# Kernel optimization log

Hardware: AMD Instinct MI355X
Metric: run time of the kernel (lower is better)

Reference implementation:

```python
import jax, jax.numpy as jnp
import numpy as np

NX, NY, NZ = 432, 496, 1
D = 64        # num_pt_features
K = 3         # NUM_K
M = 1024      # memory size
BEV = 128     # num_bev_features
NCOORD = 3
NV = 10000    # pillars in scene
NP = 16384    # points in scene
BN_EPS = 1e-3
SHRINK = 0.0025


def hard_shrink_relu(x, lambd, eps=1e-12):
    return jax.nn.relu(x - lambd) * x / (jnp.abs(x - lambd) + eps)


def batchnorm_train(x, gamma, beta, eps=BN_EPS):
    # torch BatchNorm1d training-mode math (biased variance)
    mu = jnp.mean(x, axis=0)
    var = jnp.mean((x - mu) ** 2, axis=0)
    return (x - mu) * jax.lax.rsqrt(var + eps) * gamma + beta


def pdist2(a, b, eps=1e-5):
    # sqrt(eps + |  ||a||^2 + ||b||^2 - 2 a.b |), shape [n1, n2]
    n1 = jnp.sum(a * a, axis=1, keepdims=True)
    n2 = jnp.sum(b * b, axis=1, keepdims=True)
    d2 = n1 + n2.T - 2.0 * (a @ b.T)
    return jnp.sqrt(eps + jnp.abs(d2))


def memory_lookup(x_flat, mem_w, shrink):
    # MemAE-style memory unit: softmax addressing + hard shrink + L1 renorm
    att = jax.nn.softmax(x_flat @ mem_w.T, axis=1)          # [N, M]
    att = hard_shrink_relu(att, shrink)
    att = att / jnp.maximum(jnp.sum(jnp.abs(att), axis=1, keepdims=True), 1e-12)
    return att @ mem_w                                       # [N, D]


def setup_inputs() -> dict:
    key = jax.random.key(0)
    ks = jax.random.split(key, 8)
    rng = np.random.default_rng(0)
    flat = rng.choice(NX * NY, size=NV, replace=False)       # unique BEV cells
    x = (flat % NX).astype(np.int32)
    y = (flat // NX).astype(np.int32)
    coords = jnp.asarray(np.stack([np.zeros(NV, np.int32), x, y,
                                   np.zeros(NV, np.int32)], axis=1))  # (b, x, y, z)
    pc = jax.random.uniform(ks[1], (NP, 4), dtype=jnp.float32)
    point_coords = pc * jnp.array([0.0, NX, NY, 1.0], dtype=jnp.float32)
    return {
        "pillar_features": jax.random.normal(ks[0], (NV, D), dtype=jnp.float32),
        "coords": coords,
        "point_features": jax.random.normal(ks[2], (NP, D), dtype=jnp.float32),
        "point_coords": point_coords,
        "adapt_w": jax.random.normal(ks[3], (BEV // 2, D * K), dtype=jnp.float32) * 0.05,
        "bn1_g": jnp.ones((BEV // 2,), dtype=jnp.float32),
        "bn1_b": jnp.zeros((BEV // 2,), dtype=jnp.float32),
        "weight_w": jax.random.normal(ks[4], (2, BEV // 2), dtype=jnp.float32) * 0.1,
        "bn2_g": jnp.ones((2,), dtype=jnp.float32),
        "bn2_b": jnp.zeros((2,), dtype=jnp.float32),
        "mem_w": jax.random.normal(ks[5], (M, D), dtype=jnp.float32) * 0.1,
    }


def reference(pillar_features, coords, point_features, point_coords,
              adapt_w, bn1_g, bn1_b, weight_w, bn2_g, bn2_b, mem_w):
    nv = pillar_features.shape[0]
    pillars = pillar_features.T                              # [D, nv]

    # --- coord-based retrieval: smallest-K pdist(pillar coords, point coords) ---
    dist = pdist2(coords.astype(jnp.float32), point_coords)  # [nv, np]
    _, idx_c = jax.lax.top_k(-dist, K)                       # [nv, K]
    pillars_positive_coord = point_features[idx_c]           # [nv, K, D]

    # --- feature-based retrieval: top-K of softmax(points @ pillars, axis=0) ---
    score = jax.nn.softmax(point_features @ pillars, axis=0) # [np, nv]
    _, idx_f = jax.lax.top_k(score.T, K)                     # [nv, K]
    points_positive = point_features[idx_f]                  # [nv, K, D]

    # --- memory unit on both branches ---
    out_f = memory_lookup(points_positive.reshape(nv * K, D), mem_w, SHRINK).reshape(nv, K * D)
    out_c = memory_lookup(pillars_positive_coord.reshape(nv * K, D), mem_w, SHRINK).reshape(nv, K * D)

    f = jax.nn.relu(batchnorm_train(out_f @ adapt_w.T, bn1_g, bn1_b))  # [nv, 64]
    c = jax.nn.relu(batchnorm_train(out_c @ adapt_w.T, bn1_g, bn1_b))  # [nv, 64]
    w = jax.nn.softmax(batchnorm_train(pillar_features @ weight_w.T, bn2_g, bn2_b), axis=-1)
    pillars_aug = w[:, :1] * f + w[:, 1:2] * c               # [nv, 64]
    pillars_full = jnp.concatenate([pillars, pillars_aug.T], axis=0)  # [128, nv]

    # --- scatter to BEV canvas ---
    bev_idx = coords[:, 1] + coords[:, 2] * NX + coords[:, 3]
    spatial = jnp.zeros((BEV, NX * NY), dtype=pillar_features.dtype).at[:, bev_idx].set(pillars_full)
    pind = jnp.zeros((NCOORD, NX * NY), dtype=pillar_features.dtype)
    pind = pind.at[0, bev_idx].set(coords[:, 2].astype(jnp.float32))
    pind = pind.at[1, bev_idx].set(coords[:, 3].astype(jnp.float32))
    pind = pind.at[2, bev_idx].set(coords[:, 1].astype(jnp.float32))

    spatial_features = spatial.reshape(1, BEV * NZ, NY, NX)
    spatial_indices = pind.reshape(1, NCOORD * NZ, NY, NX)
    return spatial_features, spatial_indices
```

## Files before the change

kernel.cpp:

```cpp
#include <hip/hip_runtime.h>
#include <math.h>

#define NXc 432
#define NYc 496
#define NVc 10000
#define NPc 16384
#define CELLS (NXc*NYc)
#define SHRINKc 0.0025f
#define NVPAD 10048
#define NBX 27
#define NBY 31
#define NBIN (NBX*NBY)

typedef unsigned short u16;
typedef __attribute__((ext_vector_type(8))) short s16x8;
typedef __attribute__((ext_vector_type(4))) float f32x4;

__device__ __forceinline__ unsigned med3u(unsigned a, unsigned b, unsigned c) {
    unsigned d;
    asm("v_med3_u32 %0, %1, %2, %3" : "=v"(d) : "v"(a), "v"(b), "v"(c));
    return d;
}

__device__ __forceinline__ u16 f2b(float x) {
    unsigned u = __float_as_uint(x);
    unsigned r = (u + 0x7fffu + ((u >> 16) & 1u)) >> 16;
    return (u16)r;
}

__global__ __launch_bounds__(256) void k_init(const float* __restrict__ pillar,
                                              const float* __restrict__ pfeat,
                                              const float* __restrict__ memw,
                                              const float* __restrict__ adapt,
                                              float* __restrict__ out, int n,
                                              float* __restrict__ stats,
                                              u16* __restrict__ pillarH,
                                              u16* __restrict__ pfeatH,
                                              u16* __restrict__ memwH,
                                              u16* __restrict__ memwTH,
                                              u16* __restrict__ badaptH) {
    int gid = blockIdx.x * 256 + threadIdx.x;
    float4 z = make_float4(0.f, 0.f, 0.f, 0.f);
    float4* o4 = (float4*)out;
    int n4 = n >> 2;
    for (int i = gid; i < n4; i += 1835008) o4[i] = z;
    if (gid < (n & 3)) out[n4 * 4 + gid] = 0.f;
    if (gid < 260) stats[gid] = 0.f;
    const int N1 = NVPAD * 64;
    const int N2 = N1 + NPc * 64;
    const int N3 = N2 + 65536;
    const int N4 = N3 + 65536;
    if (gid < N1) {
        int v = gid >> 6;
        pillarH[gid] = f2b(v < NVc ? pillar[gid] : 0.f);
    } else if (gid < N2) {
        pfeatH[gid - N1] = f2b(pfeat[gid - N1]);
    } else if (gid < N3) {
        memwH[gid - N2] = f2b(memw[gid - N2]);
    } else if (gid < N4) {
        int i = gid - N3;
        int d = i >> 10, j = i & 1023;
        memwTH[i] = f2b(memw[j * 64 + d]);
    } else {
        int i = gid - N4;
        int c = i >> 6, d = i & 63;
        badaptH[i] = f2b(adapt[(c & 63) * 192 + (c >> 6) * 64 + d]);
    }
}

__global__ __launch_bounds__(1024) void k_binscan(const float* __restrict__ pcoord,
                                                  int* __restrict__ binStart,
                                                  int* __restrict__ binCursor) {
    __shared__ int hcnt[1024];
    __shared__ int sc[1024];
    int t = threadIdx.x;
    hcnt[t] = 0;
    __syncthreads();
    for (int j = t; j < NPc; j += 1024) {
        float qx = pcoord[j * 4 + 1], qy = pcoord[j * 4 + 2];
        int bx = (int)(qx * 0.0625f); if (bx > NBX - 1) bx = NBX - 1;
        int by = (int)(qy * 0.0625f); if (by > NBY - 1) by = NBY - 1;
        atomicAdd(&hcnt[by * NBX + bx], 1);
    }
    __syncthreads();
    int vcount = (t < NBIN) ? hcnt[t] : 0;
    sc[t] = vcount;
    __syncthreads();
    for (int off = 1; off < 1024; off <<= 1) {
        int add = (t >= off) ? sc[t - off] : 0;
        __syncthreads();
        sc[t] += add;
        __syncthreads();
    }
    int excl = sc[t] - vcount;
    if (t <= NBIN) { binStart[t] = excl; binCursor[t] = excl; }
}

__global__ __launch_bounds__(256) void k_binfill(const float* __restrict__ pcoord,
                                                 int* __restrict__ binCursor,
                                                 float4* __restrict__ binPC) {
    int j = blockIdx.x * 256 + threadIdx.x;
    float qx = pcoord[j * 4 + 1], qy = pcoord[j * 4 + 2], qz = pcoord[j * 4 + 3];
    int bx = (int)(qx * 0.0625f); if (bx > NBX - 1) bx = NBX - 1;
    int by = (int)(qy * 0.0625f); if (by > NBY - 1) by = NBY - 1;
    int slot = atomicAdd(&binCursor[by * NBX + bx], 1);
    binPC[slot] = make_float4(qx, qy, qz * qz, __uint_as_float((unsigned)j));
}

__global__ __launch_bounds__(256) void k_dist6(const int* __restrict__ coords,
                                               const float4* __restrict__ binPC,
                                               const int* __restrict__ binStart,
                                               int* __restrict__ dIdx6) {
    int v = blockIdx.x * 256 + threadIdx.x;
    if (v >= NVc) return;
    int xi = coords[v * 4 + 1], yi = coords[v * 4 + 2];
    float x = (float)xi, y = (float)yi;
    int bx = xi >> 4; if (bx > NBX - 1) bx = NBX - 1;
    int by = yi >> 4; if (by > NBY - 1) by = NBY - 1;
    unsigned kk[6] = {~0u, ~0u, ~0u, ~0u, ~0u, ~0u};
    for (int r = 0; r < 32; ++r) {
        int x0 = bx - r, x1 = bx + r, y0 = by - r, y1 = by + r;
        for (int cy = y0; cy <= y1; ++cy) {
            if (cy < 0 || cy > NBY - 1) continue;
            int step = (cy == y0 || cy == y1) ? 1 : (x1 > x0 ? x1 - x0 : 1);
            for (int cx = x0; cx <= x1; cx += step) {
                if (cx < 0 || cx > NBX - 1) continue;
                int b = cy * NBX + cx;
                int s0 = binStart[b], s1 = binStart[b + 1];
                for (int s = s0; s < s1; ++s) {
                    float4 p = binPC[s];
                    float e1 = x - p.x, e2 = y - p.y;
                    float d2 = fmaf(e1, e1, fmaf(e2, e2, p.z));
                    unsigned t = (__float_as_uint(d2) & 0xFFFFC000u) | __float_as_uint(p.w);
                    kk[5] = med3u(kk[4], kk[5], t);
                    kk[4] = med3u(kk[3], kk[4], t);
                    kk[3] = med3u(kk[2], kk[3], t);
                    kk[2] = med3u(kk[1], kk[2], t);
                    kk[1] = med3u(kk[0], kk[1], t);
                    kk[0] = kk[0] < t ? kk[0] : t;
                }
            }
        }
        if (kk[2] != ~0u) {
            float d3 = __uint_as_float(kk[2] & 0xFFFFC000u);
            if (256.f * (float)(r * r) > d3 * 1.004f + 1e-3f) break;
        }
    }
#pragma unroll
    for (int j = 0; j < 6; ++j) dIdx6[v * 6 + j] = (int)(kk[j] & 16383u);
}

__global__ __launch_bounds__(256) void k_score5(const u16* __restrict__ pillarH,
                                                const u16* __restrict__ pfeatH,
                                                int* __restrict__ sIdx) {
    __shared__ u16 BF[2][8192];
    int t = threadIdx.x;
    int w = t >> 6, l = t & 63;
    int lm = l & 15, qd = l >> 4;
    int pb = blockIdx.x * 64;
    int cb = blockIdx.y * 1024;

    const u16* arow = pillarH + (size_t)(pb + 16 * w + lm) * 64 + qd * 8;
    s16x8 a0 = *(const s16x8*)arow;
    s16x8 a1 = *(const s16x8*)(arow + 32);

    int so[4], doff[4];
#pragma unroll
    for (int r = 0; r < 4; ++r) {
        int q = t + 256 * r;
        int row = q >> 3, g = q & 7;
        so[r] = row * 64 + g * 8;
        doff[r] = (((row >> 4) * 8 + g) * 16 + ((row & 15) ^ g)) * 8;
    }
    uint4 pre[4];
    const u16* src = pfeatH + (size_t)cb * 64;
#pragma unroll
    for (int r = 0; r < 4; ++r) pre[r] = *(const uint4*)(src + so[r]);
#pragma unroll
    for (int r = 0; r < 4; ++r) *(uint4*)&BF[0][doff[r]] = pre[r];

    unsigned sk[4][4];
#pragma unroll
    for (int r = 0; r < 4; ++r)
#pragma unroll
        for (int j = 0; j < 4; ++j) sk[r][j] = 0u;

    for (int s = 0; s < 8; ++s) {
        __syncthreads();
        if (s < 7) {
            const u16* s2 = src + (size_t)(s + 1) * 128 * 64;
#pragma unroll
            for (int r = 0; r < 4; ++r) pre[r] = *(const uint4*)(s2 + so[r]);
        }
        const u16* B = &BF[s & 1][0];
#pragma unroll
        for (int pt = 0; pt < 8; ++pt) {
            s16x8 b0 = *(const s16x8*)&B[(((pt * 8 + qd) * 16) + (lm ^ qd)) * 8];
            s16x8 b1 = *(const s16x8*)&B[(((pt * 8 + qd + 4) * 16) + (lm ^ (qd + 4))) * 8];
            f32x4 acc = {256.f, 256.f, 256.f, 256.f};
            acc = __builtin_amdgcn_mfma_f32_16x16x32_bf16(a0, b0, acc, 0, 0, 0);
            acc = __builtin_amdgcn_mfma_f32_16x16x32_bf16(a1, b1, acc, 0, 0, 0);
            unsigned idf = (unsigned)(1023 - (s * 128 + pt * 16 + lm));
#pragma unroll
            for (int r = 0; r < 4; ++r) {
                unsigned key = (__float_as_uint(acc[r]) & 0xFFFFFC00u) | idf;
                sk[r][3] = med3u(sk[r][2], sk[r][3], key);
                sk[r][2] = med3u(sk[r][1], sk[r][2], key);
                sk[r][1] = med3u(sk[r][0], sk[r][1], key);
                sk[r][0] = sk[r][0] > key ? sk[r][0] : key;
            }
        }
        if (s < 7) {
#pragma unroll
            for (int r = 0; r < 4; ++r) *(uint4*)&BF[(s + 1) & 1][doff[r]] = pre[r];
        }
    }
    __syncthreads();
    unsigned* mrg = (unsigned*)&BF[0][0];
#pragma unroll
    for (int r = 0; r < 4; ++r) {
        int row = 16 * w + qd * 4 + r;
        *(uint4*)&mrg[(row * 16 + lm) * 4] = make_uint4(sk[r][0], sk[r][1], sk[r][2], sk[r][3]);
    }
    __syncthreads();
    if (t < 64) {
        int gpr = pb + t;
        unsigned m0 = 0u, m1 = 0u, m2 = 0u, m3 = 0u;
#pragma unroll 4
        for (int cc = 0; cc < 16; ++cc) {
            uint4 v = *(const uint4*)&mrg[(t * 16 + cc) * 4];
#pragma unroll
            for (int j = 0; j < 4; ++j) {
                unsigned x = j == 0 ? v.x : (j == 1 ? v.y : (j == 2 ? v.z : v.w));
                m3 = med3u(m2, m3, x);
                m2 = med3u(m1, m2, x);
                m1 = med3u(m0, m1, x);
                m0 = m0 > x ? m0 : x;
            }
        }
        if (gpr < NVc) {
            int base = (blockIdx.y * NVc + gpr) * 4;
            sIdx[base + 0] = cb + 1023 - (int)(m0 & 1023u);
            sIdx[base + 1] = cb + 1023 - (int)(m1 & 1023u);
            sIdx[base + 2] = cb + 1023 - (int)(m2 & 1023u);
            sIdx[base + 3] = cb + 1023 - (int)(m3 & 1023u);
        }
    }
}

__global__ __launch_bounds__(256) void k_rerank(const float* __restrict__ pillar,
                                                const int* __restrict__ coords,
                                                const float* __restrict__ pfeat,
                                                const float* __restrict__ pcoord,
                                                const int* __restrict__ sIdx,
                                                const int* __restrict__ dIdx6,
                                                int* __restrict__ idx_f,
                                                int* __restrict__ idx_c) {
    int t = threadIdx.x;
    int wv = t >> 6, l = t & 63;
    int v = blockIdx.x * 4 + wv;
    int chunk = l >> 2, slot = l & 3;
    int ps = sIdx[(chunk * NVc + v) * 4 + slot];
    int pd = dIdx6[v * 6 + (l < 6 ? l : 0)];
    double s = 0.0;
#pragma unroll
    for (int i = 0; i < 16; ++i) {
        float4 a = *(const float4*)(pillar + v * 64 + 4 * i);
        float4 b = *(const float4*)(pfeat + ps * 64 + 4 * i);
        s += (double)a.x * (double)b.x + (double)a.y * (double)b.y
           + (double)a.z * (double)b.z + (double)a.w * (double)b.w;
    }
    float4 qc = *(const float4*)(pcoord + pd * 4);
    double db_ = (double)coords[v * 4 + 0] - (double)qc.x;
    double dx_ = (double)coords[v * 4 + 1] - (double)qc.y;
    double dy_ = (double)coords[v * 4 + 2] - (double)qc.z;
    double dz_ = (double)coords[v * 4 + 3] - (double)qc.w;
    double d2 = db_ * db_ + dx_ * dx_ + dy_ * dy_ + dz_ * dz_;
    double sv = s; int sx = ps;
    for (int k = 0; k < 3; ++k) {
        double bv = sv; int bi = sx;
#pragma unroll
        for (int off = 32; off >= 1; off >>= 1) {
            double ov = __shfl_xor(bv, off);
            int    oi = __shfl_xor(bi, off);
            if (ov > bv || (ov == bv && oi < bi)) { bv = ov; bi = oi; }
        }
        if (l == 0) idx_f[v * 3 + k] = bi;
        if (sx == bi) { sv = -INFINITY; sx = 0x7fffffff; }
    }
    double dv = d2; int dx2 = pd;
    for (int k = 0; k < 3; ++k) {
        double bv = dv; int bi = dx2;
#pragma unroll
        for (int off = 32; off >= 1; off >>= 1) {
            double ov = __shfl_xor(bv, off);
            int    oi = __shfl_xor(bi, off);
            if (ov < bv || (ov == bv && oi < bi)) { bv = ov; bi = oi; }
        }
        if (l == 0) idx_c[v * 3 + k] = bi;
        if (dx2 == bi) { dv = INFINITY; dx2 = 0x7fffffff; }
    }
}

__global__ __launch_bounds__(256) void k_mem2(const u16* __restrict__ pfeatH,
                                              const u16* __restrict__ memwH,
                                              const u16* __restrict__ memwTH,
                                              u16* __restrict__ PoutH) {
    __shared__ u16 WH[8192];
    __shared__ u16 WT[8192];
    __shared__ u16 ST[4][2048];
    int t = threadIdx.x;
    int w = t >> 6, l = t & 63;
    int lm = l & 15, qd = l >> 4;
    int pb = blockIdx.x * 64;

    const u16* arow = pfeatH + (size_t)(pb + 16 * w + lm) * 64 + qd * 8;
    s16x8 a0 = *(const s16x8*)arow;
    s16x8 a1 = *(const s16x8*)(arow + 32);

    float mM[4] = {-INFINITY, -INFINITY, -INFINITY, -INFINITY};
    float Zs[4] = {0.f, 0.f, 0.f, 0.f};

    for (int tile = 0; tile < 8; ++tile) {
        __syncthreads();
#pragma unroll
        for (int r = 0; r < 4; ++r) {
            int q = t + 256 * r;
            int row = q >> 3, g = q & 7;
            uint4 v = *(const uint4*)(memwH + (size_t)(tile * 128 + row) * 64 + g * 8);
            *(uint4*)&WH[(((row >> 4) * 8 + g) * 16 + ((row & 15) ^ g)) * 8] = v;
        }
        __syncthreads();
        f32x4 acc[8];
#pragma unroll
        for (int st = 0; st < 8; ++st) {
            s16x8 b0 = *(const s16x8*)&WH[((st * 8 + qd) * 16 + (lm ^ qd)) * 8];
            s16x8 b1 = *(const s16x8*)&WH[((st * 8 + qd + 4) * 16 + (lm ^ (qd + 4))) * 8];
            f32x4 z = {0.f, 0.f, 0.f, 0.f};
            z = __builtin_amdgcn_mfma_f32_16x16x32_bf16(a0, b0, z, 0, 0, 0);
            z = __builtin_amdgcn_mfma_f32_16x16x32_bf16(a1, b1, z, 0, 0, 0);
            acc[st] = z;
        }
#pragma unroll
        for (int r = 0; r < 4; ++r) {
            float tmax = acc[0][r];
#pragma unroll
            for (int st = 1; st < 8; ++st) tmax = fmaxf(tmax, acc[st][r]);
            float mn = fmaxf(mM[r], tmax);
            float zacc = Zs[r] * __expf(mM[r] - mn);
#pragma unroll
            for (int st = 0; st < 8; ++st) zacc += __expf(acc[st][r] - mn);
            mM[r] = mn; Zs[r] = zacc;
        }
    }
#pragma unroll
    for (int r = 0; r < 4; ++r) {
#pragma unroll
        for (int off = 1; off < 16; off <<= 1) {
            float om = __shfl_xor(mM[r], off);
            float oz = __shfl_xor(Zs[r], off);
            float mn = fmaxf(mM[r], om);
            Zs[r] = Zs[r] * __expf(mM[r] - mn) + oz * __expf(om - mn);
            mM[r] = mn;
        }
    }
    float invZ[4], L1[4] = {0.f, 0.f, 0.f, 0.f};
#pragma unroll
    for (int r = 0; r < 4; ++r) invZ[r] = 1.f / Zs[r];

    f32x4 oacc[4];
#pragma unroll
    for (int n = 0; n < 4; ++n) oacc[n] = (f32x4){0.f, 0.f, 0.f, 0.f};

    for (int tile = 0; tile < 8; ++tile) {
        __syncthreads();
#pragma unroll
        for (int r = 0; r < 4; ++r) {
            int q = t + 256 * r;
            int row = q >> 3, g = q & 7;
            uint4 v = *(const uint4*)(memwH + (size_t)(tile * 128 + row) * 64 + g * 8);
            *(uint4*)&WH[(((row >> 4) * 8 + g) * 16 + ((row & 15) ^ g)) * 8] = v;
        }
#pragma unroll
        for (int r = 0; r < 4; ++r) {
            int q = t + 256 * r;
            int row = q >> 4, g = q & 15;
            uint4 v = *(const uint4*)(memwTH + (size_t)row * 1024 + tile * 128 + g * 8);
            *(uint4*)&WT[(g * 64 + (row ^ g)) * 8] = v;
        }
        __syncthreads();
#pragma unroll
        for (int st = 0; st < 8; ++st) {
            s16x8 b0 = *(const s16x8*)&WH[((st * 8 + qd) * 16 + (lm ^ qd)) * 8];
            s16x8 b1 = *(const s16x8*)&WH[((st * 8 + qd + 4) * 16 + (lm ^ (qd + 4))) * 8];
            f32x4 z = {0.f, 0.f, 0.f, 0.f};
            z = __builtin_amdgcn_mfma_f32_16x16x32_bf16(a0, b0, z, 0, 0, 0);
            z = __builtin_amdgcn_mfma_f32_16x16x32_bf16(a1, b1, z, 0, 0, 0);
            int g2 = st * 2 + (lm >> 3);
#pragma unroll
            for (int r = 0; r < 4; ++r) {
                float e = __expf(z[r] - mM[r]);
                float a = e * invZ[r];
                float tt = a - SHRINKc;
                float sres = fmaxf(tt, 0.f) * a / (fabsf(tt) + 1e-12f);
                L1[r] += sres;
                int rr = qd * 4 + r;
                ST[w][(g2 * 16 + (rr ^ g2)) * 8 + (lm & 7)] = f2b(sres);
            }
        }
#pragma unroll
        for (int ks = 0; ks < 4; ++ks) {
            int g = ks * 4 + qd;
            s16x8 af = *(const s16x8*)&ST[w][(g * 16 + (lm ^ g)) * 8];
#pragma unroll
            for (int n = 0; n < 4; ++n) {
                s16x8 bf = *(const s16x8*)&WT[(g * 64 + ((n * 16 + lm) ^ g)) * 8];
                oacc[n] = __builtin_amdgcn_mfma_f32_16x16x32_bf16(af, bf, oacc[n], 0, 0, 0);
            }
        }
    }
#pragma unroll
    for (int r = 0; r < 4; ++r) {
#pragma unroll
        for (int off = 1; off < 16; off <<= 1) L1[r] += __shfl_xor(L1[r], off);
        L1[r] = 1.f / fmaxf(L1[r], 1e-12f);
    }
#pragma unroll
    for (int n = 0; n < 4; ++n)
#pragma unroll
        for (int r = 0; r < 4; ++r)
            PoutH[(size_t)(pb + 16 * w + qd * 4 + r) * 64 + n * 16 + lm] =
                f2b(oacc[n][r] * L1[r]);
}

__global__ __launch_bounds__(256) void k_proj2(const u16* __restrict__ PoutH,
                                               const u16* __restrict__ badaptH,
                                               float* __restrict__ Q) {
    __shared__ u16 AD[12288];
    int t = threadIdx.x;
    int w = t >> 6, l = t & 63;
    int lm = l & 15, qd = l >> 4;
    int pb = blockIdx.x * 64;
#pragma unroll
    for (int r = 0; r < 6; ++r) {
        int q = t + 256 * r;
        int row = q >> 3, g = q & 7;
        uint4 v = *(const uint4*)(badaptH + (size_t)row * 64 + g * 8);
        *(uint4*)&AD[(((row >> 4) * 8 + g) * 16 + ((row & 15) ^ g)) * 8] = v;
    }
    const u16* arow = PoutH + (size_t)(pb + 16 * w + lm) * 64 + qd * 8;
    s16x8 a0 = *(const s16x8*)arow;
    s16x8 a1 = *(const s16x8*)(arow + 32);
    __syncthreads();
    f32x4 acc[12];
#pragma unroll
    for (int nt = 0; nt < 12; ++nt) {
        s16x8 b0 = *(const s16x8*)&AD[(((nt * 8 + qd) * 16) + (lm ^ qd)) * 8];
        s16x8 b1 = *(const s16x8*)&AD[(((nt * 8 + qd + 4) * 16) + (lm ^ (qd + 4))) * 8];
        f32x4 z = {0.f, 0.f, 0.f, 0.f};
        z = __builtin_amdgcn_mfma_f32_16x16x32_bf16(a0, b0, z, 0, 0, 0);
        z = __builtin_amdgcn_mfma_f32_16x16x32_bf16(a1, b1, z, 0, 0, 0);
        acc[nt] = z;
    }
#pragma unroll
    for (int nt = 0; nt < 12; ++nt)
#pragma unroll
        for (int r = 0; r < 4; ++r)
            Q[(size_t)(pb + 16 * w + qd * 4 + r) * 192 + nt * 16 + lm] = acc[nt][r];
}

__global__ __launch_bounds__(256) void k_gather(const float* __restrict__ Q,
                                                const int* __restrict__ idx_f,
                                                const int* __restrict__ idx_c,
                                                const float* __restrict__ pillar,
                                                const float* __restrict__ ww,
                                                float* __restrict__ f_pre,
                                                float* __restrict__ c_pre,
                                                float* __restrict__ w_pre,
                                                float* __restrict__ stats) {
    __shared__ float red[4][4][64];
    __shared__ float redw[4][4];
    int t = threadIdx.x;
    int wv = t >> 6, l = t & 63;
    int base = blockIdx.x * 40;
    int vend = base + 40;
    float fs = 0, fq = 0, cs = 0, cq = 0, ws0 = 0, wq0 = 0, ws1 = 0, wq1 = 0;
    float w0l = ww[l], w1l = ww[64 + l];
    for (int v = base + wv; v < vend; v += 4) {
        int if0 = idx_f[v * 3], if1 = idx_f[v * 3 + 1], if2 = idx_f[v * 3 + 2];
        float f = Q[if0 * 192 + l] + Q[if1 * 192 + 64 + l] + Q[if2 * 192 + 128 + l];
        f_pre[v * 64 + l] = f; fs += f; fq += f * f;
        int ic0 = idx_c[v * 3], ic1 = idx_c[v * 3 + 1], ic2 = idx_c[v * 3 + 2];
        float c = Q[ic0 * 192 + l] + Q[ic1 * 192 + 64 + l] + Q[ic2 * 192 + 128 + l];
        c_pre[v * 64 + l] = c; cs += c; cq += c * c;
        float pv = pillar[v * 64 + l];
        float a0 = pv * w0l, a1 = pv * w1l;
#pragma unroll
        for (int off = 32; off >= 1; off >>= 1) {
            a0 += __shfl_xor(a0, off);
            a1 += __shfl_xor(a1, off);
        }
        if (l == 0) { w_pre[v * 2] = a0; w_pre[v * 2 + 1] = a1; }
        ws0 += a0; wq0 += a0 * a0; ws1 += a1; wq1 += a1 * a1;
    }
    red[0][wv][l] = fs; red[1][wv][l] = fq; red[2][wv][l] = cs; red[3][wv][l] = cq;
    if (l == 0) { redw[wv][0] = ws0; redw[wv][1] = wq0; redw[wv][2] = ws1; redw[wv][3] = wq1; }
    __syncthreads();
    if (wv == 0) {
#pragma unroll
        for (int q = 0; q < 4; ++q) {
            float sum = red[q][0][l] + red[q][1][l] + red[q][2][l] + red[q][3][l];
            atomicAdd(&stats[q * 64 + l], sum);
        }
        if (l < 4) {
            float sum = redw[0][l] + redw[1][l] + redw[2][l] + redw[3][l];
            atomicAdd(&stats[256 + l], sum);
        }
    }
}

__global__ __launch_bounds__(256) void k_final(const float* __restrict__ f_pre,
                                               const float* __restrict__ c_pre,
                                               const float* __restrict__ w_pre,
                                               const float* __restrict__ stats,
                                               const float* __restrict__ pillar,
                                               const int* __restrict__ coords,
                                               const float* __restrict__ g1,
                                               const float* __restrict__ b1,
                                               const float* __restrict__ g2,
                                               const float* __restrict__ b2,
                                               float* __restrict__ out) {
    int t = threadIdx.x;
    int wv = t >> 6, l = t & 63;
    int v = blockIdx.x * 4 + wv;
    const float invn = 1.0f / (float)NVc;
    float mf = stats[l] * invn;
    float vf = stats[64 + l] * invn - mf * mf;
    float rf = rsqrtf(vf + 1e-3f);
    float mc = stats[128 + l] * invn;
    float vc = stats[192 + l] * invn - mc * mc;
    float rc = rsqrtf(vc + 1e-3f);
    float mw0 = stats[256] * invn, vw0 = stats[257] * invn - mw0 * mw0;
    float mw1 = stats[258] * invn, vw1 = stats[259] * invn - mw1 * mw1;
    float rw0 = rsqrtf(vw0 + 1e-3f), rw1 = rsqrtf(vw1 + 1e-3f);
    float fb = (f_pre[v * 64 + l] - mf) * rf * g1[l] + b1[l];
    float f = fmaxf(fb, 0.f);
    float cb_ = (c_pre[v * 64 + l] - mc) * rc * g1[l] + b1[l];
    float c = fmaxf(cb_, 0.f);
    float z0 = (w_pre[v * 2] - mw0) * rw0 * g2[0] + b2[0];
    float z1 = (w_pre[v * 2 + 1] - mw1) * rw1 * g2[1] + b2[1];
    float mz = fmaxf(z0, z1);
    float e0 = __expf(z0 - mz), e1 = __expf(z1 - mz);
    float wd = 1.f / (e0 + e1);
    float aug = (e0 * wd) * f + (e1 * wd) * c;
    int cxi = coords[v * 4 + 1], cyi = coords[v * 4 + 2], czi = coords[v * 4 + 3];
    int cell = cxi + cyi * NXc + czi;
    out[l * CELLS + cell] = pillar[v * 64 + l];
    out[(64 + l) * CELLS + cell] = aug;
    if (l == 0) {
        float* o1 = out + 128 * CELLS;
        o1[cell] = (float)cyi;
        o1[CELLS + cell] = (float)czi;
        o1[2 * CELLS + cell] = (float)cxi;
    }
}

extern "C" void kernel_launch(void* const* d_in, const int* in_sizes, int n_in,
                              void* d_out, int out_size, void* d_ws, size_t ws_size,
                              hipStream_t stream) {
    const float* pillar = (const float*)d_in[0];
    const int*   coords = (const int*)d_in[1];
    const float* pfeat  = (const float*)d_in[2];
    const float* pcoord = (const float*)d_in[3];
    const float* adapt  = (const float*)d_in[4];
    const float* bn1g   = (const float*)d_in[5];
    const float* bn1b   = (const float*)d_in[6];
    const float* ww     = (const float*)d_in[7];
    const float* bn2g   = (const float*)d_in[8];
    const float* bn2b   = (const float*)d_in[9];
    const float* memw   = (const float*)d_in[10];
    float* out = (float*)d_out;
    float* ws  = (float*)d_ws;
    u16*   PoutH = (u16*)(ws + 0);
    float* Q     = ws + 1048576;
    int*   sIdx  = (int*)(ws + 4194304);
    int*   binStart  = (int*)(ws + 4834304);
    int*   binCursor = (int*)(ws + 4835200);
    int*   dIdx6     = (int*)(ws + 4836824);
    float4* binPC    = (float4*)(ws + 4896824);
    u16*   memwH   = (u16*)(ws + 4970000);
    u16*   memwTH  = (u16*)(ws + 5002768);
    u16*   badaptH = (u16*)(ws + 5035536);
    int*   idxf  = (int*)(ws + 5474304);
    int*   idxc  = (int*)(ws + 5504304);
    float* fpre  = ws + 5534304;
    float* cpre  = ws + 6174304;
    float* wpre  = ws + 6814304;
    float* stats = ws + 6834304;
    u16* pillarH = (u16*)(ws + 5534304);
    u16* pfeatH  = pillarH + (size_t)NVPAD * 64;

    k_init   <<<7168, 256, 0, stream>>>(pillar, pfeat, memw, adapt, out, out_size,
                                        stats, pillarH, pfeatH, memwH, memwTH, badaptH);
    k_binscan<<<1, 1024, 0, stream>>>(pcoord, binStart, binCursor);
    k_binfill<<<64, 256, 0, stream>>>(pcoord, binCursor, binPC);
    k_score5 <<<dim3(157, 16), 256, 0, stream>>>(pillarH, pfeatH, sIdx);
    k_dist6  <<<40, 256, 0, stream>>>(coords, binPC, binStart, dIdx6);
    k_rerank <<<2500, 256, 0, stream>>>(pillar, coords, pfeat, pcoord, sIdx, dIdx6, idxf, idxc);
    k_mem2   <<<256, 256, 0, stream>>>(pfeatH, memwH, memwTH, PoutH);
    k_proj2  <<<256, 256, 0, stream>>>(PoutH, badaptH, Q);
    k_gather <<<250, 256, 0, stream>>>(Q, idxf, idxc, pillar, ww, fpre, cpre, wpre, stats);
    k_final  <<<2500, 256, 0, stream>>>(fpre, cpre, wpre, stats, pillar, coords,
                                        bn1g, bn1b, bn2g, bn2b, out);
}
```

Before: 374.8 us.

## Replace canvas zero-fill plus scatter with cell-map gather that writes output once

```diff
diff --git a/kernel.cpp b/kernel.cpp
--- a/kernel.cpp
+++ b/kernel.cpp
@@ -32,19 +32,15 @@
                                               const float* __restrict__ pfeat,
                                               const float* __restrict__ memw,
                                               const float* __restrict__ adapt,
-                                              float* __restrict__ out, int n,
                                               float* __restrict__ stats,
+                                              int* __restrict__ cellMap,
                                               u16* __restrict__ pillarH,
                                               u16* __restrict__ pfeatH,
                                               u16* __restrict__ memwH,
                                               u16* __restrict__ memwTH,
                                               u16* __restrict__ badaptH) {
     int gid = blockIdx.x * 256 + threadIdx.x;
-    float4 z = make_float4(0.f, 0.f, 0.f, 0.f);
-    float4* o4 = (float4*)out;
-    int n4 = n >> 2;
-    for (int i = gid; i < n4; i += 1835008) o4[i] = z;
-    if (gid < (n & 3)) out[n4 * 4 + gid] = 0.f;
+    if (gid < CELLS) cellMap[gid] = -1;
     if (gid < 260) stats[gid] = 0.f;
     const int N1 = NVPAD * 64;
     const int N2 = N1 + NPc * 64;
@@ -97,21 +93,27 @@
 }
 
 __global__ __launch_bounds__(256) void k_binfill(const float* __restrict__ pcoord,
+                                                 const int* __restrict__ coords,
                                                  int* __restrict__ binCursor,
-                                                 float4* __restrict__ binPC) {
+                                                 float4* __restrict__ binPC,
+                                                 int* __restrict__ cellMap) {
     int j = blockIdx.x * 256 + threadIdx.x;
     float qx = pcoord[j * 4 + 1], qy = pcoord[j * 4 + 2], qz = pcoord[j * 4 + 3];
     int bx = (int)(qx * 0.0625f); if (bx > NBX - 1) bx = NBX - 1;
     int by = (int)(qy * 0.0625f); if (by > NBY - 1) by = NBY - 1;
     int slot = atomicAdd(&binCursor[by * NBX + bx], 1);
     binPC[slot] = make_float4(qx, qy, qz * qz, __uint_as_float((unsigned)j));
-}
-
-__global__ __launch_bounds__(256) void k_dist6(const int* __restrict__ coords,
-                                               const float4* __restrict__ binPC,
-                                               const int* __restrict__ binStart,
-                                               int* __restrict__ dIdx6) {
-    int v = blockIdx.x * 256 + threadIdx.x;
+    if (j < NVc) {
+        int cell = coords[j * 4 + 1] + coords[j * 4 + 2] * NXc + coords[j * 4 + 3];
+        cellMap[cell] = j;
+    }
+}
+
+__global__ __launch_bounds__(64) void k_dist6(const int* __restrict__ coords,
+                                              const float4* __restrict__ binPC,
+                                              const int* __restrict__ binStart,
+                                              int* __restrict__ dIdx6) {
+    int v = blockIdx.x * 64 + threadIdx.x;
     if (v >= NVc) return;
     int xi = coords[v * 4 + 1], yi = coords[v * 4 + 2];
     float x = (float)xi, y = (float)yi;
@@ -147,7 +149,7 @@
         }
     }
 #pragma unroll
-    for (int j = 0; j < 6; ++j) dIdx6[v * 6 + j] = (int)(kk[j] & 16383u);
+    for (int j2 = 0; j2 < 6; ++j2) dIdx6[v * 6 + j2] = (int)(kk[j2] & 16383u);
 }
 
 __global__ __launch_bounds__(256) void k_score5(const u16* __restrict__ pillarH,
@@ -519,17 +521,15 @@
     }
 }
 
-__global__ __launch_bounds__(256) void k_final(const float* __restrict__ f_pre,
-                                               const float* __restrict__ c_pre,
-                                               const float* __restrict__ w_pre,
-                                               const float* __restrict__ stats,
-                                               const float* __restrict__ pillar,
-                                               const int* __restrict__ coords,
-                                               const float* __restrict__ g1,
-                                               const float* __restrict__ b1,
-                                               const float* __restrict__ g2,
-                                               const float* __restrict__ b2,
-                                               float* __restrict__ out) {
+__global__ __launch_bounds__(256) void k_aug(const float* __restrict__ f_pre,
+                                             const float* __restrict__ c_pre,
+                                             const float* __restrict__ w_pre,
+                                             const float* __restrict__ stats,
+                                             const float* __restrict__ g1,
+                                             const float* __restrict__ b1,
+                                             const float* __restrict__ g2,
+                                             const float* __restrict__ b2,
+                                             float* __restrict__ aug) {
     int t = threadIdx.x;
     int wv = t >> 6, l = t & 63;
     int v = blockIdx.x * 4 + wv;
@@ -552,16 +552,45 @@
     float mz = fmaxf(z0, z1);
     float e0 = __expf(z0 - mz), e1 = __expf(z1 - mz);
     float wd = 1.f / (e0 + e1);
-    float aug = (e0 * wd) * f + (e1 * wd) * c;
-    int cxi = coords[v * 4 + 1], cyi = coords[v * 4 + 2], czi = coords[v * 4 + 3];
-    int cell = cxi + cyi * NXc + czi;
-    out[l * CELLS + cell] = pillar[v * 64 + l];
-    out[(64 + l) * CELLS + cell] = aug;
-    if (l == 0) {
-        float* o1 = out + 128 * CELLS;
-        o1[cell] = (float)cyi;
-        o1[CELLS + cell] = (float)czi;
-        o1[2 * CELLS + cell] = (float)cxi;
+    aug[v * 64 + l] = (e0 * wd) * f + (e1 * wd) * c;
+}
+
+__global__ __launch_bounds__(256) void k_out(const int* __restrict__ cellMap,
+                                             const float* __restrict__ pillar,
+                                             const float* __restrict__ aug,
+                                             float* __restrict__ out) {
+    int c4 = (blockIdx.x * 256 + threadIdx.x) * 4;
+    if (c4 >= CELLS) return;
+    int4 cm = *(const int4*)(cellMap + c4);
+    int f0 = blockIdx.y * 33;
+    int f1 = f0 + 33; if (f1 > 131) f1 = 131;
+    for (int f = f0; f < f1; ++f) {
+        float4 val;
+        if (f < 64) {
+            val.x = cm.x >= 0 ? pillar[cm.x * 64 + f] : 0.f;
+            val.y = cm.y >= 0 ? pillar[cm.y * 64 + f] : 0.f;
+            val.z = cm.z >= 0 ? pillar[cm.z * 64 + f] : 0.f;
+            val.w = cm.w >= 0 ? pillar[cm.w * 64 + f] : 0.f;
+        } else if (f < 128) {
+            int fa = f - 64;
+            val.x = cm.x >= 0 ? aug[cm.x * 64 + fa] : 0.f;
+            val.y = cm.y >= 0 ? aug[cm.y * 64 + fa] : 0.f;
+            val.z = cm.z >= 0 ? aug[cm.z * 64 + fa] : 0.f;
+            val.w = cm.w >= 0 ? aug[cm.w * 64 + fa] : 0.f;
+        } else if (f == 128) {
+            val.x = cm.x >= 0 ? (float)((c4 + 0) / NXc) : 0.f;
+            val.y = cm.y >= 0 ? (float)((c4 + 1) / NXc) : 0.f;
+            val.z = cm.z >= 0 ? (float)((c4 + 2) / NXc) : 0.f;
+            val.w = cm.w >= 0 ? (float)((c4 + 3) / NXc) : 0.f;
+        } else if (f == 129) {
+            val = make_float4(0.f, 0.f, 0.f, 0.f);
+        } else {
+            val.x = cm.x >= 0 ? (float)((c4 + 0) % NXc) : 0.f;
+            val.y = cm.y >= 0 ? (float)((c4 + 1) % NXc) : 0.f;
+            val.z = cm.z >= 0 ? (float)((c4 + 2) % NXc) : 0.f;
+            val.w = cm.w >= 0 ? (float)((c4 + 3) % NXc) : 0.f;
+        }
+        *(float4*)(out + (size_t)f * CELLS + c4) = val;
     }
 }
 
@@ -597,19 +626,21 @@
     float* cpre  = ws + 6174304;
     float* wpre  = ws + 6814304;
     float* stats = ws + 6834304;
+    int*   cellMap = (int*)(ws + 6840000);
+    float* aug   = ws + 7060000;
     u16* pillarH = (u16*)(ws + 5534304);
     u16* pfeatH  = pillarH + (size_t)NVPAD * 64;
 
-    k_init   <<<7168, 256, 0, stream>>>(pillar, pfeat, memw, adapt, out, out_size,
-                                        stats, pillarH, pfeatH, memwH, memwTH, badaptH);
+    k_init   <<<7168, 256, 0, stream>>>(pillar, pfeat, memw, adapt, stats, cellMap,
+                                        pillarH, pfeatH, memwH, memwTH, badaptH);
     k_binscan<<<1, 1024, 0, stream>>>(pcoord, binStart, binCursor);
-    k_binfill<<<64, 256, 0, stream>>>(pcoord, binCursor, binPC);
+    k_binfill<<<64, 256, 0, stream>>>(pcoord, coords, binCursor, binPC, cellMap);
     k_score5 <<<dim3(157, 16), 256, 0, stream>>>(pillarH, pfeatH, sIdx);
-    k_dist6  <<<40, 256, 0, stream>>>(coords, binPC, binStart, dIdx6);
+    k_dist6  <<<157, 64, 0, stream>>>(coords, binPC, binStart, dIdx6);
     k_rerank <<<2500, 256, 0, stream>>>(pillar, coords, pfeat, pcoord, sIdx, dIdx6, idxf, idxc);
     k_mem2   <<<256, 256, 0, stream>>>(pfeatH, memwH, memwTH, PoutH);
     k_proj2  <<<256, 256, 0, stream>>>(PoutH, badaptH, Q);
     k_gather <<<250, 256, 0, stream>>>(Q, idxf, idxc, pillar, ww, fpre, cpre, wpre, stats);
-    k_final  <<<2500, 256, 0, stream>>>(fpre, cpre, wpre, stats, pillar, coords,
-                                        bn1g, bn1b, bn2g, bn2b, out);
-}
+    k_aug    <<<2500, 256, 0, stream>>>(fpre, cpre, wpre, stats, bn1g, bn1b, bn2g, bn2b, aug);
+    k_out    <<<dim3(210, 4), 256, 0, stream>>>(cellMap, pillar, aug, out);
+}
```

Result: faster. 359.5 us (-4.1%).
